# Optimization experiments

Measured on AMD Instinct MI355X. Metric: run time of the kernel, lower is better.

Reference implementation:

```python
import jax, jax.numpy as jnp
import numpy as np

B, N, M = 4, 1024, 4096
DQ, DC = 1024, 1024
H, DH = 16, 64
INNER = H * DH
SCALE = DH ** -0.5


def setup_inputs() -> dict:
    key = jax.random.key(0)
    ks = jax.random.split(key, 6)
    x = jax.random.normal(ks[0], (B, N, DQ), dtype=jnp.float32)
    context = jax.random.normal(ks[1], (B, M, DC), dtype=jnp.float32)
    mask = jax.random.bernoulli(ks[2], 0.9, (B, M))  # bool, True = keep
    # weights, scaled like default torch Linear init (~1/sqrt(fan_in))
    Wq = jax.random.normal(ks[3], (DQ, INNER), dtype=jnp.float32) / np.sqrt(DQ)
    Wkv = jax.random.normal(ks[4], (DC, 2 * INNER), dtype=jnp.float32) / np.sqrt(DC)
    Wo = jax.random.normal(ks[5], (INNER, DQ), dtype=jnp.float32) / np.sqrt(INNER)
    bo = jnp.zeros((DQ,), dtype=jnp.float32)
    return {"x": x, "context": context, "mask": mask,
            "Wq": Wq, "Wkv": Wkv, "Wo": Wo, "bo": bo}


def reference(x, context, mask, Wq, Wkv, Wo, bo):
    # projections
    q = x @ Wq                     # [b, n, h*d]
    kv = context @ Wkv             # [b, m, 2*h*d]
    k, v = jnp.split(kv, 2, axis=-1)
    # split heads: [b, s, h*d] -> [b, h, s, d]
    def heads(t):
        b, s, _ = t.shape
        return t.reshape(b, s, H, DH).transpose(0, 2, 1, 3)
    q, k, v = heads(q), heads(k), heads(v)
    sim = jnp.einsum('bhid,bhjd->bhij', q, k) * SCALE   # [b, h, n, m]
    max_neg = -jnp.finfo(sim.dtype).max
    sim = jnp.where(mask[:, None, None, :], sim, max_neg)
    sim = jnp.clip(sim, -5.0, 5.0)  # masked entries become exactly -5
    attn = jax.nn.softmax(sim, axis=-1)
    out = jnp.einsum('bhij,bhjd->bhid', attn, v)        # [b, h, n, d]
    out = out.transpose(0, 2, 1, 3).reshape(x.shape[0], x.shape[1], INNER)
    return out @ Wo + bo
```

## Files before the change

kernel.cpp:

```cpp
#include <hip/hip_runtime.h>
#include <hip/hip_bf16.h>


typedef __attribute__((ext_vector_type(8))) short short8;
typedef __attribute__((ext_vector_type(8))) unsigned short u16x8;
typedef __attribute__((ext_vector_type(4))) float f32x4;
typedef __attribute__((ext_vector_type(16))) float f32x16;

static __device__ __forceinline__ void gload_lds16(const void* g, void* l) {
  __builtin_amdgcn_global_load_lds((const __attribute__((address_space(1))) void*)g,
                                   (__attribute__((address_space(3))) void*)l, 16, 0, 0);
}

static __device__ __forceinline__ unsigned short f2bf(float f) {
  __hip_bfloat16 h = __float2bfloat16(f);
  unsigned short u;
  __builtin_memcpy(&u, &h, 2);
  return u;
}

static __device__ __forceinline__ float bf2f(unsigned short u) {
  unsigned int x = (unsigned int)u << 16;
  float f;
  __builtin_memcpy(&f, &x, 4);
  return f;
}

static __device__ __forceinline__ unsigned int pack_rnd(float a, float b) {
  unsigned int ua, ub;
  __builtin_memcpy(&ua, &a, 4);
  __builtin_memcpy(&ub, &b, 4);
  return __builtin_amdgcn_perm(ua + 0x8000u, ub + 0x8000u, 0x03020706u);
}

static __device__ __forceinline__ unsigned int pack_trunc(float a, float b) {
  unsigned int ua, ub;
  __builtin_memcpy(&ua, &a, 4);
  __builtin_memcpy(&ub, &b, 4);
  return __builtin_amdgcn_perm(ua, ub, 0x03020706u);
}

__global__ __launch_bounds__(256) void cast_bf16_kernel(const float* __restrict__ in,
                                                        unsigned short* __restrict__ out,
                                                        int n8) {
  int idx = blockIdx.x * 256 + threadIdx.x;
  int stride = gridDim.x * 256;
  for (int i = idx; i < n8; i += stride) {
    const float4* p = (const float4*)in + (size_t)i * 2;
    float4 a = p[0], b = p[1];
    u16x8 r;
    r[0] = f2bf(a.x); r[1] = f2bf(a.y); r[2] = f2bf(a.z); r[3] = f2bf(a.w);
    r[4] = f2bf(b.x); r[5] = f2bf(b.y); r[6] = f2bf(b.z); r[7] = f2bf(b.w);
    *((u16x8*)out + i) = r;
  }
}

__global__ __launch_bounds__(256) void mask_bias_kernel(const int* __restrict__ mask,
                                                        float* __restrict__ bias, int n) {
  int i = blockIdx.x * 256 + threadIdx.x;
  if (i < n) bias[i] = mask[i] ? 0.0f : -1e30f;
}

__global__ __launch_bounds__(256) void transpose_cast_kernel(const float* __restrict__ W,
                                                             unsigned short* __restrict__ Wt,
                                                             int K, int N) {
  __shared__ float tile[32][33];
  int n0 = blockIdx.x * 32, k0 = blockIdx.y * 32;
  int tx = threadIdx.x & 31, ty = threadIdx.x >> 5;
#pragma unroll
  for (int r = 0; r < 32; r += 8)
    tile[ty + r][tx] = W[(size_t)(k0 + ty + r) * N + n0 + tx];
  __syncthreads();
#pragma unroll
  for (int r = 0; r < 32; r += 8)
    Wt[(size_t)(n0 + ty + r) * K + k0 + tx] = f2bf(tile[tx][ty + r]);
}

template <int EPI>
__global__ __launch_bounds__(256, 2) void gemm_bt_kernel(
    const unsigned short* __restrict__ A, const unsigned short* __restrict__ Bt,
    int M, int N, int K,
    unsigned short* __restrict__ out0,
    float* __restrict__ outF, const float* __restrict__ bias) {
  __shared__ unsigned short As[128 * 64];
  __shared__ unsigned short Bs[128 * 64];
  const int tid = threadIdx.x;
  const int l = tid & 63;
  const int lq = l & 15, g = l >> 4;
  const int w = tid >> 6;
  const int wr = w >> 1, wc = w & 1;
  const int nwg = gridDim.x * gridDim.y;
  const int idl = blockIdx.y * gridDim.x + blockIdx.x;
  const int lin = (idl & 7) * (nwg >> 3) + (idl >> 3);
  const int m0 = (lin / gridDim.x) * 128, n0 = (lin % gridDim.x) * 128;

  f32x4 acc[4][4] = {};

  for (int k0 = 0; k0 < K; k0 += 64) {
    __syncthreads();
#pragma unroll
    for (int t = 0; t < 4; ++t) {
      int c = t * 256 + tid;
      int row = c >> 3, cb = c & 7;
      int srcoff = (cb * 16) ^ ((row & 7) << 4);
      char* la = (char*)As + t * 4096 + (tid & 192) * 16;
      gload_lds16((const char*)(A + (size_t)(m0 + row) * K + k0) + srcoff, la);
      char* lb = (char*)Bs + t * 4096 + (tid & 192) * 16;
      gload_lds16((const char*)(Bt + (size_t)(n0 + row) * K + k0) + srcoff, lb);
    }
    __syncthreads();
#pragma unroll
    for (int ks = 0; ks < 2; ++ks) {
      short8 af[4], bfr[4];
#pragma unroll
      for (int mt = 0; mt < 4; ++mt) {
        int row = wr * 64 + mt * 16 + lq;
        af[mt] = *(const short8*)&As[row * 64 + ((ks * 32 + g * 8) ^ ((row & 7) << 3))];
      }
#pragma unroll
      for (int nt = 0; nt < 4; ++nt) {
        int row = wc * 64 + nt * 16 + lq;
        bfr[nt] = *(const short8*)&Bs[row * 64 + ((ks * 32 + g * 8) ^ ((row & 7) << 3))];
      }
#pragma unroll
      for (int mt = 0; mt < 4; ++mt)
#pragma unroll
        for (int nt = 0; nt < 4; ++nt)
          acc[mt][nt] =
              __builtin_amdgcn_mfma_f32_16x16x32_bf16(af[mt], bfr[nt], acc[mt][nt], 0, 0, 0);
    }
  }

#pragma unroll
  for (int mt = 0; mt < 4; ++mt) {
#pragma unroll
    for (int nt = 0; nt < 4; ++nt) {
#pragma unroll
      for (int r = 0; r < 4; ++r) {
        int row = m0 + wr * 64 + mt * 16 + g * 4 + r;
        int col = n0 + wc * 64 + nt * 16 + lq;
        float v = acc[mt][nt][r];
        if (EPI == 0) {
          int b = row >> 10, nq = row & 1023;
          int h = col >> 6, d = col & 63;
          out0[(((size_t)(b * 16 + h)) * 1024 + nq) * 64 + d] =
              f2bf(v * 0.18033688011112042f);
        } else {
          outF[(size_t)row * 1024 + col] = v + bias[col];
        }
      }
    }
  }
}

__global__ __launch_bounds__(512, 2) void gemm256_kv_kernel(
    const unsigned short* __restrict__ A, const unsigned short* __restrict__ Bt,
    unsigned short* __restrict__ K2out, unsigned short* __restrict__ V2out) {
  __shared__ unsigned short lds[4 * 16384];
  const int tid = threadIdx.x;
  const int l = tid & 63;
  const int lq = l & 15, g = l >> 4;
  const int w = tid >> 6;
  const int wr = w >> 2, wc = w & 3;
  const int nwg = gridDim.x * gridDim.y;
  const int idl = blockIdx.y * gridDim.x + blockIdx.x;
  const int lin = (idl & 7) * (nwg >> 3) + (idl >> 3);
  const int m0 = (lin / gridDim.x) * 256;
  const int n0 = (lin % gridDim.x) * 256;

  const int rA0 = tid >> 2, rA1 = (512 + tid) >> 2;
  const int ch = tid & 3;
  const unsigned short* sA0 = A + (size_t)(m0 + rA0) * 1024 + ((ch ^ (rA0 & 3)) << 3);
  const unsigned short* sA1 = A + (size_t)(m0 + rA1) * 1024 + ((ch ^ (rA1 & 3)) << 3);
  const unsigned short* sB0 = Bt + (size_t)(n0 + rA0) * 1024 + ((ch ^ (rA0 & 3)) << 3);
  const unsigned short* sB1 = Bt + (size_t)(n0 + rA1) * 1024 + ((ch ^ (rA1 & 3)) << 3);
  const int wub = (tid & 448) * 16;

  const int coff = (g ^ (lq & 3)) << 4;
  const int aoff = (wr * 128 + lq) * 64 + coff;
  const int boff = 16384 + (wc * 64 + lq) * 64 + coff;

  f32x4 acc[8][4] = {};

#define STAGE256(t_, s_)                                                   \
  do {                                                                     \
    char* _b = (char*)lds + (s_) * 32768;                                  \
    gload_lds16(sA0 + (t_) * 32, _b + wub);                                \
    gload_lds16(sA1 + (t_) * 32, _b + 8192 + wub);                         \
    gload_lds16(sB0 + (t_) * 32, _b + 16384 + wub);                        \
    gload_lds16(sB1 + (t_) * 32, _b + 24576 + wub);                        \
  } while (0)

#define COMPUTE256(s_)                                                     \
  do {                                                                     \
    const char* _pa = (const char*)lds + (s_) * 32768 + aoff;              \
    const char* _pb = (const char*)lds + (s_) * 32768 + boff;              \
    short8 af[8], bfv[4];                                                  \
    _Pragma("unroll") for (int mt = 0; mt < 8; ++mt)                       \
        af[mt] = *(const short8*)(_pa + mt * 1024);                        \
    _Pragma("unroll") for (int nt = 0; nt < 4; ++nt)                       \
        bfv[nt] = *(const short8*)(_pb + nt * 1024);                       \
    __builtin_amdgcn_s_setprio(1);                                         \
    _Pragma("unroll") for (int mt = 0; mt < 8; ++mt)                       \
        _Pragma("unroll") for (int nt = 0; nt < 4; ++nt)                   \
            acc[mt][nt] = __builtin_amdgcn_mfma_f32_16x16x32_bf16(         \
                af[mt], bfv[nt], acc[mt][nt], 0, 0, 0);                    \
    __builtin_amdgcn_s_setprio(0);                                         \
  } while (0)

#define PHASE256(vm_, dostage_, t_, s_stage_, s_comp_)                     \
  do {                                                                     \
    asm volatile("s_waitcnt vmcnt(" #vm_ ")" ::: "memory");                \
    __builtin_amdgcn_s_barrier();                                          \
    __builtin_amdgcn_sched_barrier(0);                                     \
    if (dostage_) STAGE256(t_, s_stage_);                                  \
    COMPUTE256(s_comp_);                                                   \
  } while (0)

  STAGE256(0, 0);
  STAGE256(1, 1);
  STAGE256(2, 2);

  for (int it = 0; it < 7; ++it) {
    const int t0 = it * 4;
    PHASE256(8, true, t0 + 3, 3, 0);
    PHASE256(8, true, t0 + 4, 0, 1);
    PHASE256(8, true, t0 + 5, 1, 2);
    PHASE256(8, true, t0 + 6, 2, 3);
  }
  PHASE256(8, true, 31, 3, 0);
  PHASE256(8, false, 0, 0, 1);
  PHASE256(4, false, 0, 0, 2);
  PHASE256(0, false, 0, 0, 3);

#undef PHASE256
#undef COMPUTE256
#undef STAGE256

#pragma unroll
  for (int mt = 0; mt < 8; ++mt) {
#pragma unroll
    for (int nt = 0; nt < 4; ++nt) {
      int col = n0 + wc * 64 + nt * 16 + lq;
      int rowb = m0 + wr * 128 + mt * 16 + g * 4;
      int b = rowb >> 12, mm = rowb & 4095;
      if (col < 1024) {
        int h = col >> 6, d = col & 63;
#pragma unroll
        for (int r = 0; r < 4; ++r) {
          size_t off =
              (((size_t)(b * 16 + h) * 8 + (d >> 3)) * 4096 + (mm + r)) * 8 + (d & 7);
          K2out[off] = f2bf(acc[mt][nt][r]);
        }
      } else {
        int hv = col - 1024;
        int h = hv >> 6, d = hv & 63;
        ushort4 pk;
        pk.x = f2bf(acc[mt][nt][0]);
        pk.y = f2bf(acc[mt][nt][1]);
        pk.z = f2bf(acc[mt][nt][2]);
        pk.w = f2bf(acc[mt][nt][3]);
        size_t off = (((size_t)(b * 16 + h) * 512 + (mm >> 3)) * 64 + d) * 8 + (mm & 7);
        *(ushort4*)&V2out[off] = pk;
      }
    }
  }
}

__global__ __launch_bounds__(256, 3) void attn_kernel(
    const unsigned short* __restrict__ K2, const unsigned short* __restrict__ V2,
    const unsigned short* __restrict__ Q, const float* __restrict__ maskb,
    unsigned short* __restrict__ numP, float* __restrict__ denP) {
  __shared__ unsigned short Ks[2][8 * 64 * 8];
  __shared__ unsigned short Vt[2][8 * 64 * 8];

  const int tid = threadIdx.x;
  const int l = tid & 63, w = tid >> 6;
  const int lq = l & 31;
  const int hi = l >> 5;

  const int id = blockIdx.x;
  const int xcd = id & 7;
  const int kk = id >> 3;
  const int qi = kk & 7;
  const int pr = xcd * 32 + (kk >> 3);
  const int bh = pr & 63, js = pr >> 6;
  const int b = bh >> 4;
  const int q0 = qi * 128 + w * 32;

  const unsigned short* Qh = Q + (size_t)bh * 1024 * 64;
  const unsigned short* Kh = K2 + (size_t)bh * 8 * 4096 * 8;
  const unsigned short* Vh = V2 + (size_t)bh * 512 * 64 * 8;
  const float* bb = maskb + b * 4096;

  const float CLIP2 = 7.213475204444817f;

  short8 qf[4];
#pragma unroll
  for (int kc = 0; kc < 4; ++kc)
    qf[kc] = *(const short8*)&Qh[(size_t)(q0 + lq) * 64 + kc * 16 + hi * 8];

  f32x16 oacc[2] = {};
  float den4[4] = {};

  const int jbeg = js * 16, jend = jbeg + 16;

#define STAGE_KV(bi_, j0_)                                                       \
  do {                                                                           \
    _Pragma("unroll") for (int t = 0; t < 2; ++t) {                              \
      int c = t * 256 + tid;                                                     \
      int db = c >> 6, jj = c & 63;                                              \
      int sig = (jj & 0x33) | ((jj & 4) << 1) | ((jj & 8) >> 1);                 \
      char* lk = (char*)(&Ks[bi_][0]) + t * 4096 + (tid & 192) * 16;             \
      gload_lds16((const char*)(Kh + ((size_t)db * 4096 + (j0_) + sig) * 8), lk);\
      char* lv = (char*)(&Vt[bi_][0]) + t * 4096 + (tid & 192) * 16;             \
      gload_lds16((const char*)(Vh + ((size_t)(((j0_) >> 3) + db) * 64 + jj) * 8), lv); \
    }                                                                            \
  } while (0)

  STAGE_KV(0, jbeg * 64);
  __syncthreads();

  for (int jt = jbeg; jt < jend; ++jt) {
    const int j0 = jt * 64;
    const int cur = jt & 1;
    if (jt + 1 < jend) STAGE_KV(cur ^ 1, j0 + 64);

    const unsigned short* Kc = &Ks[cur][0];
    const unsigned short* Vc = &Vt[cur][0];

    f32x16 s0, s1;
#pragma unroll
    for (int bq = 0; bq < 4; ++bq) {
      int boffm = j0 + ((bq & 1) << 2) + (hi << 3) + ((bq >> 1) << 4);
      f32x4 m4a = *(const f32x4*)&bb[boffm];
      f32x4 m4b = *(const f32x4*)&bb[boffm + 32];
#pragma unroll
      for (int e = 0; e < 4; ++e) {
        s0[bq * 4 + e] = m4a[e];
        s1[bq * 4 + e] = m4b[e];
      }
    }
    __builtin_amdgcn_s_setprio(1);
#pragma unroll
    for (int kc = 0; kc < 4; ++kc) {
      short8 kf0 = *(const short8*)((const char*)Kc + (2 * kc + hi) * 1024 + lq * 16);
      s0 = __builtin_amdgcn_mfma_f32_32x32x16_bf16(kf0, qf[kc], s0, 0, 0, 0);
    }
#pragma unroll
    for (int kc = 0; kc < 4; ++kc) {
      short8 kf1 = *(const short8*)((const char*)Kc + (2 * kc + hi) * 1024 + (32 + lq) * 16);
      s1 = __builtin_amdgcn_mfma_f32_32x32x16_bf16(kf1, qf[kc], s1, 0, 0, 0);
    }
    __builtin_amdgcn_s_setprio(0);
#pragma unroll
    for (int r = 0; r < 16; ++r) {
      float p = __builtin_amdgcn_exp2f(__builtin_amdgcn_fmed3f(s0[r], -CLIP2, CLIP2));
      den4[r & 3] += p;
      s0[r] = p;
    }
#pragma unroll
    for (int r = 0; r < 16; ++r) {
      float p = __builtin_amdgcn_exp2f(__builtin_amdgcn_fmed3f(s1[r], -CLIP2, CLIP2));
      den4[r & 3] += p;
      s1[r] = p;
    }
    unsigned int w0[8], w1[8];
#pragma unroll
    for (int i = 0; i < 8; ++i) w0[i] = pack_trunc(s0[i * 2], s0[i * 2 + 1]);
#pragma unroll
    for (int i = 0; i < 8; ++i) w1[i] = pack_trunc(s1[i * 2], s1[i * 2 + 1]);
    __builtin_amdgcn_s_setprio(1);
#pragma unroll
    for (int kt = 0; kt < 2; ++kt) {
      union { unsigned int u[4]; short8 s; } pa;
      pa.u[0] = w0[kt * 4 + 0];
      pa.u[1] = w0[kt * 4 + 1];
      pa.u[2] = w0[kt * 4 + 2];
      pa.u[3] = w0[kt * 4 + 3];
#pragma unroll
      for (int dt = 0; dt < 2; ++dt) {
        short8 vf = *(const short8*)((const char*)Vc +
            (2 * kt + hi) * 1024 + (dt * 32 + lq) * 16);
        oacc[dt] = __builtin_amdgcn_mfma_f32_32x32x16_bf16(pa.s, vf, oacc[dt], 0, 0, 0);
      }
    }
#pragma unroll
    for (int kt = 0; kt < 2; ++kt) {
      union { unsigned int u[4]; short8 s; } pa;
      pa.u[0] = w1[kt * 4 + 0];
      pa.u[1] = w1[kt * 4 + 1];
      pa.u[2] = w1[kt * 4 + 2];
      pa.u[3] = w1[kt * 4 + 3];
#pragma unroll
      for (int dt = 0; dt < 2; ++dt) {
        short8 vf = *(const short8*)((const char*)Vc +
            (4 + 2 * kt + hi) * 1024 + (dt * 32 + lq) * 16);
        oacc[dt] = __builtin_amdgcn_mfma_f32_32x32x16_bf16(pa.s, vf, oacc[dt], 0, 0, 0);
      }
    }
    __builtin_amdgcn_s_setprio(0);
    __syncthreads();
  }
#undef STAGE_KV

  float den = (den4[0] + den4[1]) + (den4[2] + den4[3]);
  den += __shfl_xor(den, 32);
  if (l < 32) denP[(((size_t)js * 64 + bh) * 1024) + q0 + l] = den;

#pragma unroll
  for (int dt = 0; dt < 2; ++dt)
#pragma unroll
    for (int r = 0; r < 16; ++r) {
      int q = q0 + (r & 3) + 8 * (r >> 2) + 4 * hi;
      int d = dt * 32 + lq;
      numP[((((size_t)js * 64 + bh) * 1024 + q) * 64) + d] = f2bf(oacc[dt][r]);
    }
}

__global__ __launch_bounds__(256) void attn_reduce_kernel(
    const unsigned short* __restrict__ numP, const float* __restrict__ denP,
    unsigned short* __restrict__ Ob) {
  int id = blockIdx.x * 256 + threadIdx.x;
  int d8 = id & 7;
  int q = (id >> 3) & 1023;
  int bh = id >> 13;
  int b = bh >> 4, h = bh & 15;
  float den = 0.f;
  float o[8] = {0.f, 0.f, 0.f, 0.f, 0.f, 0.f, 0.f, 0.f};
#pragma unroll
  for (int s = 0; s < 4; ++s) {
    const unsigned short* np =
        numP + ((((size_t)s * 64 + bh) * 1024 + q) * 64 + d8 * 8);
    u16x8 v = *(const u16x8*)np;
    den += denP[((size_t)s * 64 + bh) * 1024 + q];
#pragma unroll
    for (int e = 0; e < 8; ++e) o[e] += bf2f(v[e]);
  }
  float r = 1.0f / den;
  u16x8 outv;
#pragma unroll
  for (int e = 0; e < 8; ++e) outv[e] = f2bf(o[e] * r);
  *(u16x8*)&Ob[(((size_t)b * 1024 + q) * 1024) + h * 64 + d8 * 8] = outv;
}

extern "C" void kernel_launch(void* const* d_in, const int* in_sizes, int n_in,
                              void* d_out, int out_size, void* d_ws, size_t ws_size,
                              hipStream_t stream) {
  (void)in_sizes; (void)n_in; (void)out_size; (void)ws_size;
  const float* x    = (const float*)d_in[0];
  const float* ctx  = (const float*)d_in[1];
  const int*   mask = (const int*)d_in[2];
  const float* Wq   = (const float*)d_in[3];
  const float* Wkv  = (const float*)d_in[4];
  const float* Wo   = (const float*)d_in[5];
  const float* bo   = (const float*)d_in[6];
  float* out = (float*)d_out;

  char* ws = (char*)d_ws;
  const size_t MB = 1 << 20;
  unsigned short* numP = (unsigned short*)(ws + 0);
  float*          denP = (float*)(ws + 32 * MB);
  float*          mbias= (float*)(ws + 33 * MB);
  unsigned short* xb   = (unsigned short*)(ws + 0);
  unsigned short* cb   = (unsigned short*)(ws + 8 * MB);
  unsigned short* WqT  = (unsigned short*)(ws + 40 * MB);
  unsigned short* WkvT = (unsigned short*)(ws + 42 * MB);
  unsigned short* WoT  = (unsigned short*)(ws + 46 * MB);
  unsigned short* Qb   = (unsigned short*)(ws + 48 * MB);
  unsigned short* K2   = (unsigned short*)(ws + 56 * MB);
  unsigned short* V2   = (unsigned short*)(ws + 88 * MB);
  unsigned short* Ob   = (unsigned short*)(ws + 120 * MB);

  cast_bf16_kernel<<<2048, 256, 0, stream>>>(x, xb, (4 * 1024 * 1024) / 8);
  cast_bf16_kernel<<<2048, 256, 0, stream>>>(ctx, cb, (16 * 1024 * 1024) / 8);
  transpose_cast_kernel<<<dim3(32, 32), 256, 0, stream>>>(Wq, WqT, 1024, 1024);
  transpose_cast_kernel<<<dim3(64, 32), 256, 0, stream>>>(Wkv, WkvT, 1024, 2048);
  transpose_cast_kernel<<<dim3(32, 32), 256, 0, stream>>>(Wo, WoT, 1024, 1024);

  gemm_bt_kernel<0><<<dim3(8, 32), 256, 0, stream>>>(xb, WqT, 4096, 1024, 1024,
                                                     Qb, (float*)nullptr,
                                                     (const float*)nullptr);
  gemm256_kv_kernel<<<dim3(8, 64), 512, 0, stream>>>(cb, WkvT, K2, V2);
  mask_bias_kernel<<<64, 256, 0, stream>>>(mask, mbias, 4 * 4096);
  attn_kernel<<<2048, 256, 0, stream>>>(K2, V2, Qb, mbias, numP, denP);
  attn_reduce_kernel<<<2048, 256, 0, stream>>>(numP, denP, Ob);
  gemm_bt_kernel<2><<<dim3(8, 32), 256, 0, stream>>>(Ob, WoT, 4096, 1024, 1024,
                                                     (unsigned short*)nullptr,
                                                     out, bo);
}
```

Before: 240.2 us.

## Restructure KV projection GEMM into fine-grained 8-phase pipelined schedule with new LDS swizzle

Rewrites the K/V projection GEMM main loop. The LDS is now two 64KB slots, each holding a 64-wide K tile split into two halves. Each 32-wide K step is split into two phases over N-fragment pairs, and every phase issues one half-tile global-to-LDS load between its LDS fragment reads and its MFMA burst. A new row-pair XOR swizzle is meant to avoid LDS bank conflicts on the 16-byte fragment reads. The aim is to overlap memory traffic with MFMA work more evenly, at the cost of twice as many barriers per K step and more complex vmcnt gating.

After: 237.4 us (median of 2 runs). Within noise of the previous version (-1.2%).

```diff
diff --git a/kernel.cpp b/kernel.cpp
--- a/kernel.cpp
+++ b/kernel.cpp
@@ -24,13 +24,6 @@
   float f;
   __builtin_memcpy(&f, &x, 4);
   return f;
-}
-
-static __device__ __forceinline__ unsigned int pack_rnd(float a, float b) {
-  unsigned int ua, ub;
-  __builtin_memcpy(&ua, &a, 4);
-  __builtin_memcpy(&ub, &b, 4);
-  return __builtin_amdgcn_perm(ua + 0x8000u, ub + 0x8000u, 0x03020706u);
 }
 
 static __device__ __forceinline__ unsigned int pack_trunc(float a, float b) {
@@ -153,96 +146,131 @@
   }
 }
 
-__global__ __launch_bounds__(512, 2) void gemm256_kv_kernel(
+__global__ __launch_bounds__(512, 2) void gemm256_kv8_kernel(
     const unsigned short* __restrict__ A, const unsigned short* __restrict__ Bt,
     unsigned short* __restrict__ K2out, unsigned short* __restrict__ V2out) {
-  __shared__ unsigned short lds[4 * 16384];
+  __shared__ unsigned short lds[65536];
   const int tid = threadIdx.x;
   const int l = tid & 63;
   const int lq = l & 15, g = l >> 4;
   const int w = tid >> 6;
-  const int wr = w >> 2, wc = w & 3;
+  const int wm = w >> 2, wn = w & 3;
   const int nwg = gridDim.x * gridDim.y;
   const int idl = blockIdx.y * gridDim.x + blockIdx.x;
   const int lin = (idl & 7) * (nwg >> 3) + (idl >> 3);
   const int m0 = (lin / gridDim.x) * 256;
   const int n0 = (lin % gridDim.x) * 256;
 
-  const int rA0 = tid >> 2, rA1 = (512 + tid) >> 2;
-  const int ch = tid & 3;
-  const unsigned short* sA0 = A + (size_t)(m0 + rA0) * 1024 + ((ch ^ (rA0 & 3)) << 3);
-  const unsigned short* sA1 = A + (size_t)(m0 + rA1) * 1024 + ((ch ^ (rA1 & 3)) << 3);
-  const unsigned short* sB0 = Bt + (size_t)(n0 + rA0) * 1024 + ((ch ^ (rA0 & 3)) << 3);
-  const unsigned short* sB1 = Bt + (size_t)(n0 + rA1) * 1024 + ((ch ^ (rA1 & 3)) << 3);
+  int row0, gg0, row1, gg1;
+  { int u = tid;       int p = u >> 3; int t = (u & 7) ^ (p & 7); row0 = 2 * p + (t >> 2); gg0 = t & 3; }
+  { int u = 512 + tid; int p = u >> 3; int t = (u & 7) ^ (p & 7); row1 = 2 * p + (t >> 2); gg1 = t & 3; }
+  const unsigned short* sA0 = A  + (size_t)(m0 + row0) * 1024 + gg0 * 8;
+  const unsigned short* sA1 = A  + (size_t)(m0 + row1) * 1024 + gg1 * 8;
+  const unsigned short* sB0 = Bt + (size_t)(n0 + row0) * 1024 + gg0 * 8;
+  const unsigned short* sB1 = Bt + (size_t)(n0 + row1) * 1024 + gg1 * 8;
   const int wub = (tid & 448) * 16;
 
-  const int coff = (g ^ (lq & 3)) << 4;
-  const int aoff = (wr * 128 + lq) * 64 + coff;
-  const int boff = 16384 + (wc * 64 + lq) * 64 + coff;
+  int aoffb[8], boffb[4];
+#pragma unroll
+  for (int mf = 0; mf < 8; ++mf) {
+    int row = wm * 128 + mf * 16 + lq;
+    int p = row >> 1;
+    int pos = (((row & 1) << 2) + g) ^ (p & 7);
+    aoffb[mf] = p * 128 + pos * 16;
+  }
+#pragma unroll
+  for (int nf = 0; nf < 4; ++nf) {
+    int row = wn * 64 + nf * 16 + lq;
+    int p = row >> 1;
+    int pos = (((row & 1) << 2) + g) ^ (p & 7);
+    boffb[nf] = 32768 + p * 128 + pos * 16;
+  }
 
   f32x4 acc[8][4] = {};
-
-#define STAGE256(t_, s_)                                                   \
-  do {                                                                     \
-    char* _b = (char*)lds + (s_) * 32768;                                  \
-    gload_lds16(sA0 + (t_) * 32, _b + wub);                                \
-    gload_lds16(sA1 + (t_) * 32, _b + 8192 + wub);                         \
-    gload_lds16(sB0 + (t_) * 32, _b + 16384 + wub);                        \
-    gload_lds16(sB1 + (t_) * 32, _b + 24576 + wub);                        \
+  short8 af[8];
+
+#define STGA(kt_, ks_, slot_)                                                      \
+  do {                                                                             \
+    gload_lds16(sA0 + (kt_) * 64 + (ks_) * 32,                                     \
+                (char*)lds + (slot_) * 65536 + (ks_) * 16384 + wub);               \
+    gload_lds16(sA1 + (kt_) * 64 + (ks_) * 32,                                     \
+                (char*)lds + (slot_) * 65536 + (ks_) * 16384 + 8192 + wub);        \
   } while (0)
-
-#define COMPUTE256(s_)                                                     \
-  do {                                                                     \
-    const char* _pa = (const char*)lds + (s_) * 32768 + aoff;              \
-    const char* _pb = (const char*)lds + (s_) * 32768 + boff;              \
-    short8 af[8], bfv[4];                                                  \
-    _Pragma("unroll") for (int mt = 0; mt < 8; ++mt)                       \
-        af[mt] = *(const short8*)(_pa + mt * 1024);                        \
-    _Pragma("unroll") for (int nt = 0; nt < 4; ++nt)                       \
-        bfv[nt] = *(const short8*)(_pb + nt * 1024);                       \
-    __builtin_amdgcn_s_setprio(1);                                         \
-    _Pragma("unroll") for (int mt = 0; mt < 8; ++mt)                       \
-        _Pragma("unroll") for (int nt = 0; nt < 4; ++nt)                   \
-            acc[mt][nt] = __builtin_amdgcn_mfma_f32_16x16x32_bf16(         \
-                af[mt], bfv[nt], acc[mt][nt], 0, 0, 0);                    \
-    __builtin_amdgcn_s_setprio(0);                                         \
+#define STGB(kt_, ks_, slot_)                                                      \
+  do {                                                                             \
+    gload_lds16(sB0 + (kt_) * 64 + (ks_) * 32,                                     \
+                (char*)lds + (slot_) * 65536 + 32768 + (ks_) * 16384 + wub);       \
+    gload_lds16(sB1 + (kt_) * 64 + (ks_) * 32,                                     \
+                (char*)lds + (slot_) * 65536 + 32768 + (ks_) * 16384 + 8192 + wub);\
   } while (0)
 
-#define PHASE256(vm_, dostage_, t_, s_stage_, s_comp_)                     \
-  do {                                                                     \
-    asm volatile("s_waitcnt vmcnt(" #vm_ ")" ::: "memory");                \
-    __builtin_amdgcn_s_barrier();                                          \
-    __builtin_amdgcn_sched_barrier(0);                                     \
-    if (dostage_) STAGE256(t_, s_stage_);                                  \
-    COMPUTE256(s_comp_);                                                   \
+#define PHASE(slot_, ks_, nfp_, RELA_, STGSTMT, GATESTMT)                          \
+  do {                                                                             \
+    const char* base_ = (const char*)lds + (slot_) * 65536 + (ks_) * 16384;        \
+    if (RELA_) {                                                                   \
+      _Pragma("unroll") for (int mf_ = 0; mf_ < 8; ++mf_)                          \
+          af[mf_] = *(const short8*)(base_ + aoffb[mf_]);                          \
+    }                                                                              \
+    short8 bf0_ = *(const short8*)(base_ + boffb[2 * (nfp_) + 0]);                 \
+    short8 bf1_ = *(const short8*)(base_ + boffb[2 * (nfp_) + 1]);                 \
+    STGSTMT;                                                                       \
+    __builtin_amdgcn_s_barrier();                                                  \
+    asm volatile("s_waitcnt lgkmcnt(0)" ::: "memory");                             \
+    __builtin_amdgcn_sched_barrier(0);                                             \
+    __builtin_amdgcn_s_setprio(1);                                                 \
+    _Pragma("unroll") for (int mf_ = 0; mf_ < 8; ++mf_) {                          \
+      acc[mf_][2 * (nfp_) + 0] = __builtin_amdgcn_mfma_f32_16x16x32_bf16(          \
+          af[mf_], bf0_, acc[mf_][2 * (nfp_) + 0], 0, 0, 0);                       \
+      acc[mf_][2 * (nfp_) + 1] = __builtin_amdgcn_mfma_f32_16x16x32_bf16(          \
+          af[mf_], bf1_, acc[mf_][2 * (nfp_) + 1], 0, 0, 0);                       \
+    }                                                                              \
+    __builtin_amdgcn_s_setprio(0);                                                 \
+    GATESTMT;                                                                      \
+    __builtin_amdgcn_s_barrier();                                                  \
   } while (0)
 
-  STAGE256(0, 0);
-  STAGE256(1, 1);
-  STAGE256(2, 2);
+#define GATE4 asm volatile("s_waitcnt vmcnt(4)" ::: "memory")
+#define GATE0 asm volatile("s_waitcnt vmcnt(0)" ::: "memory")
+#define NOSTMT do {} while (0)
+
+  STGA(0, 0, 0); STGA(0, 1, 0); STGB(0, 0, 0); STGB(0, 1, 0);
+  STGA(1, 0, 1); STGB(1, 0, 1);
+  GATE4;
+  __builtin_amdgcn_s_barrier();
 
   for (int it = 0; it < 7; ++it) {
-    const int t0 = it * 4;
-    PHASE256(8, true, t0 + 3, 3, 0);
-    PHASE256(8, true, t0 + 4, 0, 1);
-    PHASE256(8, true, t0 + 5, 1, 2);
-    PHASE256(8, true, t0 + 6, 2, 3);
-  }
-  PHASE256(8, true, 31, 3, 0);
-  PHASE256(8, false, 0, 0, 1);
-  PHASE256(4, false, 0, 0, 2);
-  PHASE256(0, false, 0, 0, 3);
-
-#undef PHASE256
-#undef COMPUTE256
-#undef STAGE256
+    const int kt = 2 * it;
+    PHASE(0, 0, 0, 1, STGA(kt + 1, 1, 1), NOSTMT);
+    PHASE(0, 0, 1, 0, STGB(kt + 1, 1, 1), NOSTMT);
+    PHASE(0, 1, 0, 1, STGA(kt + 2, 0, 0), NOSTMT);
+    PHASE(0, 1, 1, 0, STGB(kt + 2, 0, 0), GATE4);
+    PHASE(1, 0, 0, 1, STGA(kt + 2, 1, 0), NOSTMT);
+    PHASE(1, 0, 1, 0, STGB(kt + 2, 1, 0), NOSTMT);
+    PHASE(1, 1, 0, 1, STGA(kt + 3, 0, 1), NOSTMT);
+    PHASE(1, 1, 1, 0, STGB(kt + 3, 0, 1), GATE4);
+  }
+  PHASE(0, 0, 0, 1, STGA(15, 1, 1), NOSTMT);
+  PHASE(0, 0, 1, 0, STGB(15, 1, 1), NOSTMT);
+  PHASE(0, 1, 0, 1, NOSTMT, NOSTMT);
+  PHASE(0, 1, 1, 0, NOSTMT, GATE0);
+  PHASE(1, 0, 0, 1, NOSTMT, NOSTMT);
+  PHASE(1, 0, 1, 0, NOSTMT, NOSTMT);
+  PHASE(1, 1, 0, 1, NOSTMT, NOSTMT);
+  PHASE(1, 1, 1, 0, NOSTMT, NOSTMT);
+
+#undef PHASE
+#undef STGA
+#undef STGB
+#undef GATE4
+#undef GATE0
+#undef NOSTMT
 
 #pragma unroll
   for (int mt = 0; mt < 8; ++mt) {
 #pragma unroll
     for (int nt = 0; nt < 4; ++nt) {
-      int col = n0 + wc * 64 + nt * 16 + lq;
-      int rowb = m0 + wr * 128 + mt * 16 + g * 4;
+      int col = n0 + wn * 64 + nt * 16 + lq;
+      int rowb = m0 + wm * 128 + mt * 16 + g * 4;
       int b = rowb >> 12, mm = rowb & 4095;
       if (col < 1024) {
         int h = col >> 6, d = col & 63;
@@ -481,7 +509,7 @@
   gemm_bt_kernel<0><<<dim3(8, 32), 256, 0, stream>>>(xb, WqT, 4096, 1024, 1024,
                                                      Qb, (float*)nullptr,
                                                      (const float*)nullptr);
-  gemm256_kv_kernel<<<dim3(8, 64), 512, 0, stream>>>(cb, WkvT, K2, V2);
+  gemm256_kv8_kernel<<<dim3(8, 64), 512, 0, stream>>>(cb, WkvT, K2, V2);
   mask_bias_kernel<<<64, 256, 0, stream>>>(mask, mbias, 4 * 4096);
   attn_kernel<<<2048, 256, 0, stream>>>(K2, V2, Qb, mbias, numP, denP);
   attn_reduce_kernel<<<2048, 256, 0, stream>>>(numP, denP, Ob);
```
